# Performance work log

Hardware: AMD Instinct MI355X
Metric: run time of the kernel (lower is better)

The kernel has to match this reference:

```python
import jax, jax.numpy as jnp
import numpy as np

B, T, D, H = 128, 512, 256, 256


def setup_inputs() -> dict:
    key = jax.random.key(0)
    k1, k2, k3, k4 = jax.random.split(key, 4)
    x = jax.random.normal(k1, (B, T, D), dtype=jnp.float32)
    x_len = jax.random.randint(k2, (B,), 1, T + 1)  # lengths in [1, T]
    W_ih = jax.random.normal(k3, (4 * H, D), dtype=jnp.float32) * 0.05
    W_hh = jax.random.normal(k4, (4 * H, H), dtype=jnp.float32) * 0.05
    b_ih = jnp.zeros((4 * H,), dtype=jnp.float32)
    # reset_params: bias_hh forget-gate chunk (index 1 of i,f,g,o) set to 1
    b_hh = jnp.zeros((4 * H,), dtype=jnp.float32).at[H:2 * H].set(1.0)
    return {"x": x, "x_len": x_len, "W_ih": W_ih, "W_hh": W_hh,
            "b_ih": b_ih, "b_hh": b_hh}


def reference(x, x_len, W_ih, W_hh, b_ih, b_hh):
    # Dropout is identity in eval mode. The sort/pack/unpack pipeline is
    # mathematically equivalent to running a masked LSTM over the padded
    # batch and zeroing outputs at positions t >= x_len (pad_packed_sequence
    # zero-pads), since output at t < len only depends on steps <= t.
    Bx, Tx, _ = x.shape
    Hh = W_hh.shape[1]
    # Precompute input projections for all timesteps: [B, T, 4H] -> [T, B, 4H]
    xg = jnp.einsum('btd,gd->btg', x, W_ih) + b_ih + b_hh
    xg = jnp.swapaxes(xg, 0, 1)

    def step(carry, xt):
        h, c = carry
        gates = xt + h @ W_hh.T  # [B, 4H]
        i, f, g, o = jnp.split(gates, 4, axis=-1)
        i = jax.nn.sigmoid(i)
        f = jax.nn.sigmoid(f)
        g = jnp.tanh(g)
        o = jax.nn.sigmoid(o)
        c = f * c + i * g
        h = o * jnp.tanh(c)
        return (h, c), h

    h0 = jnp.zeros((Bx, Hh), x.dtype)
    (_, _), hs = jax.lax.scan(step, (h0, h0), xg)  # hs: [T, B, H]
    out = jnp.swapaxes(hs, 0, 1)  # [B, T, H]
    mask = jnp.arange(Tx)[None, :] < x_len[:, None]  # [B, T]
    return jnp.where(mask[..., None], out, jnp.zeros((), x.dtype))
```

## Files before the change

kernel.cpp:

```cpp
#include <hip/hip_runtime.h>
#include <hip/hip_fp16.h>
#include <math.h>

#define BB 128
#define TT 512
#define DD 256
#define HH 256
#define NG 1024

typedef _Float16 h2_t __attribute__((ext_vector_type(2)));
typedef _Float16 f16x8 __attribute__((ext_vector_type(8)));
typedef float f32x4 __attribute__((ext_vector_type(4)));

#if __has_builtin(__builtin_amdgcn_fdot2)
__device__ __forceinline__ float fdot2_(h2_t a, h2_t b, float c) {
    return __builtin_amdgcn_fdot2(a, b, c, false);
}
#else
__device__ __forceinline__ float fdot2_(h2_t a, h2_t b, float c) {
    return c + (float)a.x * (float)b.x + (float)a.y * (float)b.y;
}
#endif

__device__ __forceinline__ float sigmoidf_(float x) {
    return 1.0f / (1.0f + __expf(-x));
}
__device__ __forceinline__ float tanhf_(float x) {
    x = fminf(15.0f, fmaxf(-15.0f, x));
    float e = __expf(2.0f * x);
    return (e - 1.0f) / (e + 1.0f);
}
__device__ __forceinline__ void dot4_(float4& acc, uint4 u, h2_t h) {
    acc.x = fdot2_(__builtin_bit_cast(h2_t, u.x), h, acc.x);
    acc.y = fdot2_(__builtin_bit_cast(h2_t, u.y), h, acc.y);
    acc.z = fdot2_(__builtin_bit_cast(h2_t, u.z), h, acc.z);
    acc.w = fdot2_(__builtin_bit_cast(h2_t, u.w), h, acc.w);
}

#if __has_builtin(__builtin_amdgcn_update_dpp)
__device__ __forceinline__ float pair_sum_(float v) {
    int x = __builtin_bit_cast(int, v);
    int y = __builtin_amdgcn_update_dpp(0, x, 0xB1, 0xF, 0xF, true);
    return v + __builtin_bit_cast(float, y);
}
#else
__device__ __forceinline__ float pair_sum_(float v) {
    return v + __shfl_xor(v, 1, 64);
}
#endif

__global__ void pack2(const float* __restrict__ W_ih, const float* __restrict__ W_hh,
                      const float* __restrict__ b_ih, const float* __restrict__ b_hh,
                      __half* __restrict__ Wg16, __half* __restrict__ Wi16,
                      __half* __restrict__ Wh16, float* __restrict__ bias_p) {
    int idx = blockIdx.x * 256 + threadIdx.x;
    int n = idx >> 8;
    int k = idx & 255;
    int g = (n & 3) * 256 + (n >> 2);
    float wih = W_ih[g * 256 + k];
    float whh = W_hh[g * 256 + k];
    Wg16[n * 256 + k] = __float2half(wih);
    size_t hidx = ((size_t)(k >> 1) * 1024 + n) * 2 + (k & 1);
    Wi16[hidx] = __float2half(wih);
    Wh16[hidx] = __float2half(whh);
    if (idx < 1024) {
        int gg = (idx & 3) * 256 + (idx >> 2);
        bias_p[idx] = b_ih[gg] + b_hh[gg];
    }
}

__global__ __launch_bounds__(256) void cvt_x(const float* __restrict__ X,
                                             __half* __restrict__ X16) {
    size_t i = ((size_t)blockIdx.x * 256 + threadIdx.x) * 8;
    float4 a = *(const float4*)&X[i];
    float4 b = *(const float4*)&X[i + 4];
    f16x8 v;
    v[0] = (_Float16)a.x; v[1] = (_Float16)a.y; v[2] = (_Float16)a.z; v[3] = (_Float16)a.w;
    v[4] = (_Float16)b.x; v[5] = (_Float16)b.y; v[6] = (_Float16)b.z; v[7] = (_Float16)b.w;
    *(f16x8*)&X16[i] = v;
}

__global__ __launch_bounds__(256) void xg_gemm_mfma(const __half* __restrict__ X16,
                                                    const __half* __restrict__ Wg16,
                                                    const float* __restrict__ bias_p,
                                                    __half* __restrict__ xg,
                                                    int t0, int lTc, int tcMask) {
    __shared__ __align__(16) __half st[4][16][72];
    int tid = threadIdx.x;
    int w = tid >> 6, lane = tid & 63;
    int row16 = lane & 15, quad = lane >> 4;
    int m0 = blockIdx.x * 64 + w * 16;
    int n0 = blockIdx.y * 64;

    int mrow = m0 + row16;
    size_t xrow = (size_t)(mrow >> lTc) * 512 + t0 + (mrow & tcMask);
    const __half* aptr = X16 + xrow * 256 + quad * 8;
    f16x8 afrag[8];
#pragma unroll
    for (int kk = 0; kk < 8; ++kk)
        afrag[kk] = *(const f16x8*)(aptr + kk * 32);

#pragma unroll
    for (int cg = 0; cg < 4; ++cg) {
        int n = n0 + cg * 16 + row16;
        const __half* bptr = Wg16 + (size_t)n * 256 + quad * 8;
        f32x4 acc = {0.0f, 0.0f, 0.0f, 0.0f};
#pragma unroll
        for (int kk = 0; kk < 8; ++kk) {
            f16x8 bfrag = *(const f16x8*)(bptr + kk * 32);
            acc = __builtin_amdgcn_mfma_f32_16x16x32_f16(afrag[kk], bfrag, acc, 0, 0, 0);
        }
        float bias = bias_p[n];
#pragma unroll
        for (int r = 0; r < 4; ++r)
            st[w][quad * 4 + r][cg * 16 + row16] = __float2half(acc[r] + bias);
    }
    __syncthreads();
    int ml = lane >> 2, cq = lane & 3;
    int mout = blockIdx.x * 64 + w * 16 + ml;
    const uint4* src = (const uint4*)&st[w][ml][cq * 16];
    uint4 v0 = src[0], v1 = src[1];
    *(uint4*)&xg[(size_t)mout * 1024 + n0 + cq * 16] = v0;
    *(uint4*)&xg[(size_t)mout * 1024 + n0 + cq * 16 + 8] = v1;
}

__global__ __launch_bounds__(512, 2) void lstm_rec4(const __half* __restrict__ xg,
                                                    const __half* __restrict__ Wh16,
                                                    const int* __restrict__ x_len,
                                                    float* __restrict__ out,
                                                    __half* __restrict__ h_state,
                                                    float* __restrict__ c_state,
                                                    int t0, int Tc) {
    __shared__ __align__(16) uint4 lw[8192];
    __shared__ __align__(16) __half hs[2][256];
    int tid = threadIdx.x;
    int c = tid >> 1, kh = tid & 1;
    int b = blockIdx.x;
    int len = x_len[b];
    const uint4* W4 = (const uint4*)Wh16;

    for (int j = tid; j < 8192; j += 512) {
        int i2 = j >> 9, kh2 = (j >> 8) & 1, c2 = j & 255;
        lw[j] = W4[(size_t)(kh2 * 64 + 44 + i2) * 256 + c2];
    }
    const uint4* wp = W4 + (size_t)(kh * 64) * 256 + c;
    uint4 wreg[44];
#pragma unroll
    for (int i = 0; i < 44; ++i) wreg[i] = wp[(size_t)i * 256];

    float cst = 0.0f;
    float hlast = 0.0f;
    if (t0 != 0) cst = c_state[b * 256 + c];
    if (kh == 0)
        hs[0][c] = (t0 == 0) ? __float2half(0.0f) : h_state[b * 256 + c];

    const __half* xgb = xg + (size_t)b * Tc * 1024 + 4 * c;
    float* outb = out + ((size_t)b * 512 + t0) * 256 + c;
    const uint4* lwb = lw + kh * 256 + c;
    __syncthreads();

    for (int tt = 0; tt < Tc; ++tt) {
        uint4 s0 = wp[(size_t)60 * 256];
        uint4 s1 = wp[(size_t)61 * 256];
        uint4 s2 = wp[(size_t)62 * 256];
        uint4 s3 = wp[(size_t)63 * 256];
        uint2 xr = *(const uint2*)(xgb + (size_t)tt * 1024);

        const uint4* h4 = (const uint4*)hs[tt & 1] + kh * 16;
        float4 acc = {0.0f, 0.0f, 0.0f, 0.0f};
#pragma unroll
        for (int j = 0; j < 11; ++j) {
            uint4 hv = h4[j];
            dot4_(acc, wreg[j * 4 + 0], __builtin_bit_cast(h2_t, hv.x));
            dot4_(acc, wreg[j * 4 + 1], __builtin_bit_cast(h2_t, hv.y));
            dot4_(acc, wreg[j * 4 + 2], __builtin_bit_cast(h2_t, hv.z));
            dot4_(acc, wreg[j * 4 + 3], __builtin_bit_cast(h2_t, hv.w));
        }
#pragma unroll
        for (int j = 11; j < 15; ++j) {
            uint4 hv = h4[j];
            int i0 = (j - 11) * 4;
            dot4_(acc, lwb[(i0 + 0) * 512], __builtin_bit_cast(h2_t, hv.x));
            dot4_(acc, lwb[(i0 + 1) * 512], __builtin_bit_cast(h2_t, hv.y));
            dot4_(acc, lwb[(i0 + 2) * 512], __builtin_bit_cast(h2_t, hv.z));
            dot4_(acc, lwb[(i0 + 3) * 512], __builtin_bit_cast(h2_t, hv.w));
        }
        {
            uint4 hv = h4[15];
            dot4_(acc, s0, __builtin_bit_cast(h2_t, hv.x));
            dot4_(acc, s1, __builtin_bit_cast(h2_t, hv.y));
            dot4_(acc, s2, __builtin_bit_cast(h2_t, hv.z));
            dot4_(acc, s3, __builtin_bit_cast(h2_t, hv.w));
        }
        float gi = pair_sum_(acc.x);
        float gf = pair_sum_(acc.y);
        float gg = pair_sum_(acc.z);
        float go = pair_sum_(acc.w);
        h2_t x01 = __builtin_bit_cast(h2_t, xr.x);
        h2_t x23 = __builtin_bit_cast(h2_t, xr.y);
        gi += (float)x01.x;
        gf += (float)x01.y;
        gg += (float)x23.x;
        go += (float)x23.y;
        float iv = sigmoidf_(gi), fv = sigmoidf_(gf);
        float gv = tanhf_(gg),   ov = sigmoidf_(go);
        cst = fv * cst + iv * gv;
        float h = ov * tanhf_(cst);
        hlast = h;
        if (kh == 0) {
            outb[(size_t)tt * 256] = (t0 + tt < len) ? h : 0.0f;
            hs[(tt & 1) ^ 1][c] = __float2half(h);
        }
        __syncthreads();
    }
    if (kh == 0) {
        h_state[b * 256 + c] = __float2half(hlast);
        c_state[b * 256 + c] = cst;
    }
}

__global__ __launch_bounds__(1024) void lstm_fused16(const float* __restrict__ X,
                                                     const __half* __restrict__ Wi16,
                                                     const __half* __restrict__ Wh16,
                                                     const float* __restrict__ bias_p,
                                                     const int* __restrict__ x_len,
                                                     float* __restrict__ out) {
    __shared__ __half hs_h[256];
    __shared__ __half xs_h[256];
    __shared__ float4 part[3][256];
    int tid = threadIdx.x;
    int c = tid & 255, kh = tid >> 8;
    int b = blockIdx.x;
    int len = x_len[b];
    float cst = 0.0f;
    float4 bias;
    if (kh == 0) {
        bias = *(const float4*)&bias_p[4 * c];
        hs_h[c] = __float2half(0.0f);
    }
    const uint4* wph = (const uint4*)(Wh16 + (size_t)(kh * 32) * 2048 + 8 * c);
    const uint4* wpi = (const uint4*)(Wi16 + (size_t)(kh * 32) * 2048 + 8 * c);
    float* outb = out + (size_t)b * 512 * 256 + c;
    __syncthreads();

    for (int t = 0; t < TT; ++t) {
        if (tid < 128) {
            float2 xv = *(const float2*)&X[((size_t)b * 512 + t) * 256 + 2 * tid];
            h2_t xh = {(_Float16)xv.x, (_Float16)xv.y};
            ((h2_t*)xs_h)[tid] = xh;
        }
        __syncthreads();
        float4 acc = {0.0f, 0.0f, 0.0f, 0.0f};
#pragma unroll 4
        for (int i = 0; i < 32; ++i) {
            uint4 uh = wph[(size_t)i * 256];
            uint4 ui = wpi[(size_t)i * 256];
            h2_t hv = ((const h2_t*)hs_h)[kh * 32 + i];
            h2_t xv = ((const h2_t*)xs_h)[kh * 32 + i];
            dot4_(acc, uh, hv);
            dot4_(acc, ui, xv);
        }
        if (kh) part[kh - 1][c] = acc;
        __syncthreads();
        if (kh == 0) {
            float4 p0 = part[0][c], p1 = part[1][c], p2 = part[2][c];
            float gi = acc.x + p0.x + p1.x + p2.x + bias.x;
            float gf = acc.y + p0.y + p1.y + p2.y + bias.y;
            float gg = acc.z + p0.z + p1.z + p2.z + bias.z;
            float go = acc.w + p0.w + p1.w + p2.w + bias.w;
            float iv = sigmoidf_(gi), fv = sigmoidf_(gf);
            float gv = tanhf_(gg),   ov = sigmoidf_(go);
            cst = fv * cst + iv * gv;
            float h = ov * tanhf_(cst);
            outb[(size_t)t * 256] = (t < len) ? h : 0.0f;
            hs_h[c] = __float2half(h);
        }
        __syncthreads();
    }
}

extern "C" void kernel_launch(void* const* d_in, const int* in_sizes, int n_in,
                              void* d_out, int out_size, void* d_ws, size_t ws_size,
                              hipStream_t stream) {
    const float* x     = (const float*)d_in[0];
    const int*   x_len = (const int*)d_in[1];
    const float* W_ih  = (const float*)d_in[2];
    const float* W_hh  = (const float*)d_in[3];
    const float* b_ih  = (const float*)d_in[4];
    const float* b_hh  = (const float*)d_in[5];
    float* out = (float*)d_out;

    char* ws = (char*)d_ws;
    __half* Wh16    = (__half*)(ws);
    __half* Wi16    = (__half*)(ws + 0x080000);
    __half* Wg16    = (__half*)(ws + 0x100000);
    float*  bias_p  = (float*)(ws + 0x180000);
    __half* h_state = (__half*)(ws + 0x181000);
    float*  c_state = (float*)(ws + 0x191000);
    __half* x16     = (__half*)(ws + 0x1B1000);
    size_t  o_xg    = 0x1B1000 + (size_t)0x2004000;
    __half* xg      = (__half*)(ws + o_xg);

    int Tc = 0;
    for (int cand = 512; cand >= 16; cand >>= 1)
        if (ws_size >= o_xg + (size_t)cand * 262144) { Tc = cand; break; }

    pack2<<<1024, 256, 0, stream>>>(W_ih, W_hh, b_ih, b_hh,
                                    Wg16, Wi16, Wh16, bias_p);
    if (Tc) {
        cvt_x<<<8192, 256, 0, stream>>>(x, x16);
        int lTc = 31 - __builtin_clz((unsigned)Tc);
        for (int t0 = 0; t0 < TT; t0 += Tc) {
            dim3 g(2 * Tc, 16);
            xg_gemm_mfma<<<g, 256, 0, stream>>>(x16, Wg16, bias_p, xg,
                                                t0, lTc, Tc - 1);
            lstm_rec4<<<BB, 512, 0, stream>>>(xg, Wh16, x_len, out,
                                              h_state, c_state, t0, Tc);
        }
    } else {
        lstm_fused16<<<BB, 1024, 0, stream>>>(x, Wi16, Wh16, bias_p, x_len, out);
    }
}
```

Baseline: 1.258 ms.

## Pin recurrent weights in AGPRs and rebalance register/LDS/global weight split

Recurrent weight rows held per thread now sit in accumulation registers, read back through v_accvgpr_read, which frees VGPRs. The register share drops from 44 to 32 uint4, the LDS share grows to 19 rows with a kh-interleaved layout, and the per-step global reload grows from 4 to 13 rows. The h buffer is padded so the two kh halves hit different LDS banks. The goal is to relieve register pressure and LDS bank conflicts, at the cost of more global/L2 reads every timestep plus the extra accvgpr read instructions.

```diff
diff --git a/kernel.cpp b/kernel.cpp
--- a/kernel.cpp
+++ b/kernel.cpp
@@ -35,6 +35,19 @@
     acc.y = fdot2_(__builtin_bit_cast(h2_t, u.y), h, acc.y);
     acc.z = fdot2_(__builtin_bit_cast(h2_t, u.z), h, acc.z);
     acc.w = fdot2_(__builtin_bit_cast(h2_t, u.w), h, acc.w);
+}
+
+__device__ __forceinline__ uint ar_(const uint& a) {
+    uint v;
+    asm volatile("v_accvgpr_read_b32 %0, %1" : "=v"(v) : "a"(a));
+    return v;
+}
+__device__ __forceinline__ void dot4a_(float4& acc, const uint4& w, h2_t h) {
+    uint ux = ar_(w.x), uy = ar_(w.y), uz = ar_(w.z), uw = ar_(w.w);
+    acc.x = fdot2_(__builtin_bit_cast(h2_t, ux), h, acc.x);
+    acc.y = fdot2_(__builtin_bit_cast(h2_t, uy), h, acc.y);
+    acc.z = fdot2_(__builtin_bit_cast(h2_t, uz), h, acc.z);
+    acc.w = fdot2_(__builtin_bit_cast(h2_t, uw), h, acc.w);
 }
 
 #if __has_builtin(__builtin_amdgcn_update_dpp)
@@ -131,66 +144,103 @@
                                                     __half* __restrict__ h_state,
                                                     float* __restrict__ c_state,
                                                     int t0, int Tc) {
-    __shared__ __align__(16) uint4 lw[8192];
-    __shared__ __align__(16) __half hs[2][256];
+    __shared__ __align__(16) uint4 lw[9728];
+    __shared__ __align__(16) __half hs[2][272];
     int tid = threadIdx.x;
     int c = tid >> 1, kh = tid & 1;
     int b = blockIdx.x;
     int len = x_len[b];
     const uint4* W4 = (const uint4*)Wh16;
 
-    for (int j = tid; j < 8192; j += 512) {
-        int i2 = j >> 9, kh2 = (j >> 8) & 1, c2 = j & 255;
-        lw[j] = W4[(size_t)(kh2 * 64 + 44 + i2) * 256 + c2];
+    for (int j = tid; j < 9728; j += 512) {
+        int i2 = j >> 9, c2 = (j >> 1) & 255, kh2 = j & 1;
+        lw[j] = W4[(size_t)(kh2 * 64 + 32 + i2) * 256 + c2];
     }
     const uint4* wp = W4 + (size_t)(kh * 64) * 256 + c;
-    uint4 wreg[44];
-#pragma unroll
-    for (int i = 0; i < 44; ++i) wreg[i] = wp[(size_t)i * 256];
+    uint4 wreg[32];
+#pragma unroll
+    for (int i = 0; i < 32; ++i) wreg[i] = wp[(size_t)i * 256];
+#define PIN4(i) asm volatile("" : "+a"(wreg[i].x), "+a"(wreg[i].y), "+a"(wreg[i].z), "+a"(wreg[i].w))
+    PIN4(0);  PIN4(1);  PIN4(2);  PIN4(3);  PIN4(4);  PIN4(5);  PIN4(6);  PIN4(7);
+    PIN4(8);  PIN4(9);  PIN4(10); PIN4(11); PIN4(12); PIN4(13); PIN4(14); PIN4(15);
+    PIN4(16); PIN4(17); PIN4(18); PIN4(19); PIN4(20); PIN4(21); PIN4(22); PIN4(23);
+    PIN4(24); PIN4(25); PIN4(26); PIN4(27); PIN4(28); PIN4(29); PIN4(30); PIN4(31);
+#undef PIN4
 
     float cst = 0.0f;
     float hlast = 0.0f;
     if (t0 != 0) cst = c_state[b * 256 + c];
     if (kh == 0)
-        hs[0][c] = (t0 == 0) ? __float2half(0.0f) : h_state[b * 256 + c];
+        hs[0][c + ((c >> 7) << 4)] = (t0 == 0) ? __float2half(0.0f)
+                                               : h_state[b * 256 + c];
 
     const __half* xgb = xg + (size_t)b * Tc * 1024 + 4 * c;
     float* outb = out + ((size_t)b * 512 + t0) * 256 + c;
-    const uint4* lwb = lw + kh * 256 + c;
+    const uint4* lwb = lw + tid;
     __syncthreads();
 
     for (int tt = 0; tt < Tc; ++tt) {
-        uint4 s0 = wp[(size_t)60 * 256];
-        uint4 s1 = wp[(size_t)61 * 256];
-        uint4 s2 = wp[(size_t)62 * 256];
-        uint4 s3 = wp[(size_t)63 * 256];
+        uint4 s0  = wp[(size_t)51 * 256];
+        uint4 s1  = wp[(size_t)52 * 256];
+        uint4 s2  = wp[(size_t)53 * 256];
+        uint4 s3  = wp[(size_t)54 * 256];
+        uint4 s4  = wp[(size_t)55 * 256];
+        uint4 s5  = wp[(size_t)56 * 256];
+        uint4 s6  = wp[(size_t)57 * 256];
+        uint4 s7  = wp[(size_t)58 * 256];
+        uint4 s8  = wp[(size_t)59 * 256];
+        uint4 s9  = wp[(size_t)60 * 256];
+        uint4 s10 = wp[(size_t)61 * 256];
+        uint4 s11 = wp[(size_t)62 * 256];
+        uint4 s12 = wp[(size_t)63 * 256];
         uint2 xr = *(const uint2*)(xgb + (size_t)tt * 1024);
 
-        const uint4* h4 = (const uint4*)hs[tt & 1] + kh * 16;
+        const uint4* h4 = (const uint4*)(hs[tt & 1]) + kh * 18;
         float4 acc = {0.0f, 0.0f, 0.0f, 0.0f};
 #pragma unroll
-        for (int j = 0; j < 11; ++j) {
+        for (int j = 0; j < 8; ++j) {
             uint4 hv = h4[j];
-            dot4_(acc, wreg[j * 4 + 0], __builtin_bit_cast(h2_t, hv.x));
-            dot4_(acc, wreg[j * 4 + 1], __builtin_bit_cast(h2_t, hv.y));
-            dot4_(acc, wreg[j * 4 + 2], __builtin_bit_cast(h2_t, hv.z));
-            dot4_(acc, wreg[j * 4 + 3], __builtin_bit_cast(h2_t, hv.w));
-        }
-#pragma unroll
-        for (int j = 11; j < 15; ++j) {
+            dot4a_(acc, wreg[j * 4 + 0], __builtin_bit_cast(h2_t, hv.x));
+            dot4a_(acc, wreg[j * 4 + 1], __builtin_bit_cast(h2_t, hv.y));
+            dot4a_(acc, wreg[j * 4 + 2], __builtin_bit_cast(h2_t, hv.z));
+            dot4a_(acc, wreg[j * 4 + 3], __builtin_bit_cast(h2_t, hv.w));
+        }
+#pragma unroll
+        for (int j = 8; j < 12; ++j) {
             uint4 hv = h4[j];
-            int i0 = (j - 11) * 4;
+            int i0 = (j - 8) * 4;
             dot4_(acc, lwb[(i0 + 0) * 512], __builtin_bit_cast(h2_t, hv.x));
             dot4_(acc, lwb[(i0 + 1) * 512], __builtin_bit_cast(h2_t, hv.y));
             dot4_(acc, lwb[(i0 + 2) * 512], __builtin_bit_cast(h2_t, hv.z));
             dot4_(acc, lwb[(i0 + 3) * 512], __builtin_bit_cast(h2_t, hv.w));
         }
         {
+            uint4 hv = h4[12];
+            dot4_(acc, lwb[16 * 512], __builtin_bit_cast(h2_t, hv.x));
+            dot4_(acc, lwb[17 * 512], __builtin_bit_cast(h2_t, hv.y));
+            dot4_(acc, lwb[18 * 512], __builtin_bit_cast(h2_t, hv.z));
+            dot4_(acc, s0, __builtin_bit_cast(h2_t, hv.w));
+        }
+        {
+            uint4 hv = h4[13];
+            dot4_(acc, s1, __builtin_bit_cast(h2_t, hv.x));
+            dot4_(acc, s2, __builtin_bit_cast(h2_t, hv.y));
+            dot4_(acc, s3, __builtin_bit_cast(h2_t, hv.z));
+            dot4_(acc, s4, __builtin_bit_cast(h2_t, hv.w));
+        }
+        {
+            uint4 hv = h4[14];
+            dot4_(acc, s5, __builtin_bit_cast(h2_t, hv.x));
+            dot4_(acc, s6, __builtin_bit_cast(h2_t, hv.y));
+            dot4_(acc, s7, __builtin_bit_cast(h2_t, hv.z));
+            dot4_(acc, s8, __builtin_bit_cast(h2_t, hv.w));
+        }
+        {
             uint4 hv = h4[15];
-            dot4_(acc, s0, __builtin_bit_cast(h2_t, hv.x));
-            dot4_(acc, s1, __builtin_bit_cast(h2_t, hv.y));
-            dot4_(acc, s2, __builtin_bit_cast(h2_t, hv.z));
-            dot4_(acc, s3, __builtin_bit_cast(h2_t, hv.w));
+            dot4_(acc, s9, __builtin_bit_cast(h2_t, hv.x));
+            dot4_(acc, s10, __builtin_bit_cast(h2_t, hv.y));
+            dot4_(acc, s11, __builtin_bit_cast(h2_t, hv.z));
+            dot4_(acc, s12, __builtin_bit_cast(h2_t, hv.w));
         }
         float gi = pair_sum_(acc.x);
         float gf = pair_sum_(acc.y);
@@ -209,7 +259,7 @@
         hlast = h;
         if (kh == 0) {
             outb[(size_t)tt * 256] = (t0 + tt < len) ? h : 0.0f;
-            hs[(tt & 1) ^ 1][c] = __float2half(h);
+            hs[(tt & 1) ^ 1][c + ((c >> 7) << 4)] = __float2half(h);
         }
         __syncthreads();
     }
```

After: 1.501 ms. 19.3% more time.

## Split LSTM recurrence K-dim across four threads per hidden unit with 1024-thread blocks

Applied to the files above, without the earlier changes.

The recurrent kernel now assigns four threads per hidden unit, each covering a quarter of the hidden dimension, instead of two, and launches 1024 threads per block. Per-thread weight storage drops from 44 registers plus LDS plus streamed loads to 12 registers, 8 LDS slots and 12 streamed global loads. The streamed loads are interleaved with the compute to hide latency. Partial sums are combined with a two-stage DPP quad reduction. This shortens the serial dot-product chain per timestep, at the cost of more threads contending at each per-step block barrier and more global weight reads per step.

```diff
diff --git a/kernel.cpp b/kernel.cpp
--- a/kernel.cpp
+++ b/kernel.cpp
@@ -38,14 +38,18 @@
 }
 
 #if __has_builtin(__builtin_amdgcn_update_dpp)
-__device__ __forceinline__ float pair_sum_(float v) {
+__device__ __forceinline__ float quad_sum_(float v) {
     int x = __builtin_bit_cast(int, v);
     int y = __builtin_amdgcn_update_dpp(0, x, 0xB1, 0xF, 0xF, true);
-    return v + __builtin_bit_cast(float, y);
+    float s = v + __builtin_bit_cast(float, y);
+    int x2 = __builtin_bit_cast(int, s);
+    int y2 = __builtin_amdgcn_update_dpp(0, x2, 0x4E, 0xF, 0xF, true);
+    return s + __builtin_bit_cast(float, y2);
 }
 #else
-__device__ __forceinline__ float pair_sum_(float v) {
-    return v + __shfl_xor(v, 1, 64);
+__device__ __forceinline__ float quad_sum_(float v) {
+    float s = v + __shfl_xor(v, 1, 64);
+    return s + __shfl_xor(s, 2, 64);
 }
 #endif
 
@@ -124,78 +128,105 @@
     *(uint4*)&xg[(size_t)mout * 1024 + n0 + cq * 16 + 8] = v1;
 }
 
-__global__ __launch_bounds__(512, 2) void lstm_rec4(const __half* __restrict__ xg,
-                                                    const __half* __restrict__ Wh16,
-                                                    const int* __restrict__ x_len,
-                                                    float* __restrict__ out,
-                                                    __half* __restrict__ h_state,
-                                                    float* __restrict__ c_state,
-                                                    int t0, int Tc) {
+__global__ __launch_bounds__(1024, 4) void lstm_rec4(const __half* __restrict__ xg,
+                                                     const __half* __restrict__ Wh16,
+                                                     const int* __restrict__ x_len,
+                                                     float* __restrict__ out,
+                                                     __half* __restrict__ h_state,
+                                                     float* __restrict__ c_state,
+                                                     int t0, int Tc) {
     __shared__ __align__(16) uint4 lw[8192];
     __shared__ __align__(16) __half hs[2][256];
     int tid = threadIdx.x;
-    int c = tid >> 1, kh = tid & 1;
+    int c = tid >> 2, kq = tid & 3;
     int b = blockIdx.x;
     int len = x_len[b];
     const uint4* W4 = (const uint4*)Wh16;
 
-    for (int j = tid; j < 8192; j += 512) {
-        int i2 = j >> 9, kh2 = (j >> 8) & 1, c2 = j & 255;
-        lw[j] = W4[(size_t)(kh2 * 64 + 44 + i2) * 256 + c2];
-    }
-    const uint4* wp = W4 + (size_t)(kh * 64) * 256 + c;
-    uint4 wreg[44];
-#pragma unroll
-    for (int i = 0; i < 44; ++i) wreg[i] = wp[(size_t)i * 256];
+    for (int j = tid; j < 8192; j += 1024) {
+        int i2 = j >> 10, r = j & 1023, c2 = r >> 2, kq2 = r & 3;
+        lw[j] = W4[(size_t)(kq2 * 32 + 12 + i2) * 256 + c2];
+    }
+    const uint4* wp = W4 + (size_t)(kq * 32) * 256 + c;
+    uint4 wreg[12];
+#pragma unroll
+    for (int i = 0; i < 12; ++i) wreg[i] = wp[(size_t)i * 256];
 
     float cst = 0.0f;
     float hlast = 0.0f;
     if (t0 != 0) cst = c_state[b * 256 + c];
-    if (kh == 0)
-        hs[0][c] = (t0 == 0) ? __float2half(0.0f) : h_state[b * 256 + c];
+    if (tid < 256)
+        hs[0][tid] = (t0 == 0) ? __float2half(0.0f) : h_state[b * 256 + tid];
 
     const __half* xgb = xg + (size_t)b * Tc * 1024 + 4 * c;
     float* outb = out + ((size_t)b * 512 + t0) * 256 + c;
-    const uint4* lwb = lw + kh * 256 + c;
+    const uint4* lwb = lw + tid;
     __syncthreads();
 
     for (int tt = 0; tt < Tc; ++tt) {
-        uint4 s0 = wp[(size_t)60 * 256];
-        uint4 s1 = wp[(size_t)61 * 256];
-        uint4 s2 = wp[(size_t)62 * 256];
-        uint4 s3 = wp[(size_t)63 * 256];
+        uint4 sA0 = wp[(size_t)20 * 256];
+        uint4 sA1 = wp[(size_t)21 * 256];
+        uint4 sA2 = wp[(size_t)22 * 256];
+        uint4 sA3 = wp[(size_t)23 * 256];
         uint2 xr = *(const uint2*)(xgb + (size_t)tt * 1024);
 
-        const uint4* h4 = (const uint4*)hs[tt & 1] + kh * 16;
+        const uint4* h4 = (const uint4*)(hs[tt & 1]) + kq * 8;
         float4 acc = {0.0f, 0.0f, 0.0f, 0.0f};
 #pragma unroll
-        for (int j = 0; j < 11; ++j) {
+        for (int j = 0; j < 3; ++j) {
             uint4 hv = h4[j];
             dot4_(acc, wreg[j * 4 + 0], __builtin_bit_cast(h2_t, hv.x));
             dot4_(acc, wreg[j * 4 + 1], __builtin_bit_cast(h2_t, hv.y));
             dot4_(acc, wreg[j * 4 + 2], __builtin_bit_cast(h2_t, hv.z));
             dot4_(acc, wreg[j * 4 + 3], __builtin_bit_cast(h2_t, hv.w));
         }
-#pragma unroll
-        for (int j = 11; j < 15; ++j) {
-            uint4 hv = h4[j];
-            int i0 = (j - 11) * 4;
-            dot4_(acc, lwb[(i0 + 0) * 512], __builtin_bit_cast(h2_t, hv.x));
-            dot4_(acc, lwb[(i0 + 1) * 512], __builtin_bit_cast(h2_t, hv.y));
-            dot4_(acc, lwb[(i0 + 2) * 512], __builtin_bit_cast(h2_t, hv.z));
-            dot4_(acc, lwb[(i0 + 3) * 512], __builtin_bit_cast(h2_t, hv.w));
-        }
-        {
-            uint4 hv = h4[15];
-            dot4_(acc, s0, __builtin_bit_cast(h2_t, hv.x));
-            dot4_(acc, s1, __builtin_bit_cast(h2_t, hv.y));
-            dot4_(acc, s2, __builtin_bit_cast(h2_t, hv.z));
-            dot4_(acc, s3, __builtin_bit_cast(h2_t, hv.w));
-        }
-        float gi = pair_sum_(acc.x);
-        float gf = pair_sum_(acc.y);
-        float gg = pair_sum_(acc.z);
-        float go = pair_sum_(acc.w);
+        uint4 sB0 = wp[(size_t)24 * 256];
+        uint4 sB1 = wp[(size_t)25 * 256];
+        uint4 sB2 = wp[(size_t)26 * 256];
+        uint4 sB3 = wp[(size_t)27 * 256];
+        {
+            uint4 hv = h4[3];
+            dot4_(acc, lwb[0 * 1024], __builtin_bit_cast(h2_t, hv.x));
+            dot4_(acc, lwb[1 * 1024], __builtin_bit_cast(h2_t, hv.y));
+            dot4_(acc, lwb[2 * 1024], __builtin_bit_cast(h2_t, hv.z));
+            dot4_(acc, lwb[3 * 1024], __builtin_bit_cast(h2_t, hv.w));
+        }
+        uint4 sC0 = wp[(size_t)28 * 256];
+        uint4 sC1 = wp[(size_t)29 * 256];
+        uint4 sC2 = wp[(size_t)30 * 256];
+        uint4 sC3 = wp[(size_t)31 * 256];
+        {
+            uint4 hv = h4[4];
+            dot4_(acc, lwb[4 * 1024], __builtin_bit_cast(h2_t, hv.x));
+            dot4_(acc, lwb[5 * 1024], __builtin_bit_cast(h2_t, hv.y));
+            dot4_(acc, lwb[6 * 1024], __builtin_bit_cast(h2_t, hv.z));
+            dot4_(acc, lwb[7 * 1024], __builtin_bit_cast(h2_t, hv.w));
+        }
+        {
+            uint4 hv = h4[5];
+            dot4_(acc, sA0, __builtin_bit_cast(h2_t, hv.x));
+            dot4_(acc, sA1, __builtin_bit_cast(h2_t, hv.y));
+            dot4_(acc, sA2, __builtin_bit_cast(h2_t, hv.z));
+            dot4_(acc, sA3, __builtin_bit_cast(h2_t, hv.w));
+        }
+        {
+            uint4 hv = h4[6];
+            dot4_(acc, sB0, __builtin_bit_cast(h2_t, hv.x));
+            dot4_(acc, sB1, __builtin_bit_cast(h2_t, hv.y));
+            dot4_(acc, sB2, __builtin_bit_cast(h2_t, hv.z));
+            dot4_(acc, sB3, __builtin_bit_cast(h2_t, hv.w));
+        }
+        {
+            uint4 hv = h4[7];
+            dot4_(acc, sC0, __builtin_bit_cast(h2_t, hv.x));
+            dot4_(acc, sC1, __builtin_bit_cast(h2_t, hv.y));
+            dot4_(acc, sC2, __builtin_bit_cast(h2_t, hv.z));
+            dot4_(acc, sC3, __builtin_bit_cast(h2_t, hv.w));
+        }
+        float gi = quad_sum_(acc.x);
+        float gf = quad_sum_(acc.y);
+        float gg = quad_sum_(acc.z);
+        float go = quad_sum_(acc.w);
         h2_t x01 = __builtin_bit_cast(h2_t, xr.x);
         h2_t x23 = __builtin_bit_cast(h2_t, xr.y);
         gi += (float)x01.x;
@@ -207,13 +238,13 @@
         cst = fv * cst + iv * gv;
         float h = ov * tanhf_(cst);
         hlast = h;
-        if (kh == 0) {
+        if (kq == 0) {
             outb[(size_t)tt * 256] = (t0 + tt < len) ? h : 0.0f;
             hs[(tt & 1) ^ 1][c] = __float2half(h);
         }
         __syncthreads();
     }
-    if (kh == 0) {
+    if (kq == 0) {
         h_state[b * 256 + c] = __float2half(hlast);
         c_state[b * 256 + c] = cst;
     }
@@ -314,8 +345,8 @@
             dim3 g(2 * Tc, 16);
             xg_gemm_mfma<<<g, 256, 0, stream>>>(x16, Wg16, bias_p, xg,
                                                 t0, lTc, Tc - 1);
-            lstm_rec4<<<BB, 512, 0, stream>>>(xg, Wh16, x_len, out,
-                                              h_state, c_state, t0, Tc);
+            lstm_rec4<<<BB, 1024, 0, stream>>>(xg, Wh16, x_len, out,
+                                               h_state, c_state, t0, Tc);
         }
     } else {
         lstm_fused16<<<BB, 1024, 0, stream>>>(x, Wi16, Wh16, bias_p, x_len, out);
```

Measured after the change: 1.493 ms. 18.7% more time.
